# Optimization experiments

Measured on AMD Instinct MI355X. Metric: run time of the kernel, lower is better.

## Reference

```python
import jax, jax.numpy as jnp
import numpy as np

N = 200_000
E = 3_200_000
H = 24

def setup_inputs() -> dict:
    key = jax.random.key(0)
    ks = jax.random.split(key, 12)
    s = 1.0 / np.sqrt(H).astype(np.float32)
    u = lambda k, shape: jax.random.uniform(k, shape, jnp.float32, -s, s)
    return {
        "x": jax.random.normal(ks[0], (N,), jnp.float32),
        "h0": jax.random.normal(ks[1], (1, N, H), jnp.float32) * 0.1,
        "c0": jax.random.normal(ks[2], (1, N, H), jnp.float32) * 0.1,
        "edge_index": jax.random.randint(ks[3], (2, E), 0, N, dtype=jnp.int32),
        "w_ih": u(ks[4], (4 * H, 1)),
        "w_hh": u(ks[5], (4 * H, H)),
        "b_ih": u(ks[6], (4 * H,)),
        "b_hh": u(ks[7], (4 * H,)),
        "gcn_w": u(ks[8], (H, H)),
        "gcn_b": u(ks[9], (H,)),
        "lin_w": u(ks[10], (1, H)),
        "lin_b": u(ks[11], (1,)),
    }

def reference(x, h0, c0, edge_index, w_ih, w_hh, b_ih, b_hh, gcn_w, gcn_b, lin_w, lin_b):
    # --- LSTM single step (seq_len=1, batch=N, input_size=1, hidden=H) ---
    h_prev = h0[0]  # [N, H]
    c_prev = c0[0]  # [N, H]
    # gates in torch order: input, forget, cell(g), output
    gates = x[:, None] * w_ih[:, 0][None, :] + b_ih + h_prev @ w_hh.T + b_hh  # [N, 4H]
    i, f, g, o = jnp.split(gates, 4, axis=-1)
    i = jax.nn.sigmoid(i); f = jax.nn.sigmoid(f); o = jax.nn.sigmoid(o); g = jnp.tanh(g)
    c = f * c_prev + i * g
    h = o * jnp.tanh(c)  # [N, H] -- LSTM output == new hidden state

    # --- GCNConv(24,24): symmetric norm with self loops (PyG default) ---
    xw = h @ gcn_w.T  # [N, H]
    src, dst = edge_index[0], edge_index[1]
    deg = jax.ops.segment_sum(jnp.ones(src.shape, xw.dtype), dst, num_segments=N) + 1.0
    dinv = jax.lax.rsqrt(deg)                      # deg >= 1 due to self loops
    norm = dinv[src] * dinv[dst]                   # [E]
    msg = xw[src] * norm[:, None]                  # [E, H]
    agg = jax.ops.segment_sum(msg, dst, num_segments=N)
    agg = agg + xw * (dinv * dinv)[:, None]        # self-loop edges
    conv = agg + gcn_b                             # [N, H]

    # --- Linear(24,1) + elementwise gate ---
    out = (conv @ lin_w.T + lin_b).reshape(-1)     # [N]
    return x * out, h[None], c[None]
```

## Files before the change

kernel.cpp:

```cpp
#include <hip/hip_runtime.h>
#include <math.h>

#define H 24
#define B0 4096
#define B0_SHIFT 12
#define MAXNB 64
#define NBPAD 65
#define REP 4
#define P 8
#define CAP 70000
#define K1_EPB 4096
#define EPT (K1_EPB / 256)

__device__ __forceinline__ float sigmoidf_(float v) {
    return 1.0f / (1.0f + __expf(-v));
}
__device__ __forceinline__ float tanhf_(float v) {
    return 1.0f - 2.0f / (__expf(2.0f * v) + 1.0f);
}

__global__ void init_kernel(unsigned* __restrict__ cursors,
                            const float* __restrict__ gcn_w,
                            const float* __restrict__ gcn_b,
                            const float* __restrict__ lin_w,
                            const float* __restrict__ lin_b,
                            float* __restrict__ g, float* __restrict__ cb, int NB) {
    int t = threadIdx.x;
    if (t < H) {
        float acc = 0.0f;
        for (int j = 0; j < H; j++) acc = fmaf(lin_w[j], gcn_w[j * H + t], acc);
        g[t] = acc;
    }
    if (t == 32) {
        float c = lin_b[0];
        for (int j = 0; j < H; j++) c = fmaf(gcn_b[j], lin_w[j], c);
        *cb = c;
    }
    if (t < MAXNB) cursors[t] = (unsigned)t * CAP;
}

__global__ __launch_bounds__(256) void scatter_kernel(
    const int* __restrict__ src, const int* __restrict__ dst,
    unsigned* __restrict__ cursors, unsigned* __restrict__ pedge, int E, int NB)
{
    __shared__ unsigned cnt[REP * NBPAD];
    __shared__ unsigned rbase[MAXNB];
    __shared__ unsigned c3[MAXNB];
    int start = blockIdx.x * K1_EPB;
    int end   = start + K1_EPB; if (end > E) end = E;
    int rep = threadIdx.x & (REP - 1);

    for (int i = threadIdx.x; i < REP * NBPAD; i += 256) cnt[i] = 0;
    __syncthreads();

    unsigned dreg[EPT];
    #pragma unroll
    for (int q = 0; q < EPT; q++) {
        int e = start + q * 256 + threadIdx.x;
        if (e < end) {
            unsigned d = (unsigned)dst[e];
            dreg[q] = d;
            atomicAdd(&cnt[rep * NBPAD + (d >> B0_SHIFT)], 1u);
        }
    }
    __syncthreads();

    for (int i = threadIdx.x; i < NB; i += 256) {
        unsigned tot = cnt[i] + cnt[NBPAD + i] + cnt[2 * NBPAD + i] + cnt[3 * NBPAD + i];
        rbase[i] = tot ? atomicAdd(&cursors[i], tot) : 0u;
        c3[i] = 0;
    }
    __syncthreads();

    #pragma unroll
    for (int q = 0; q < EPT; q++) {
        int e = start + q * 256 + threadIdx.x;
        if (e < end) {
            unsigned d = dreg[q];
            unsigned b = d >> B0_SHIFT;
            unsigned slot = atomicAdd(&c3[b], 1u);
            unsigned idx  = rbase[b] + slot;
            if (idx < (b + 1u) * CAP)
                pedge[idx] = ((unsigned)src[e] << B0_SHIFT) | (d & (B0 - 1));
        }
    }
}

__global__ __launch_bounds__(256) void deghist_kernel(
    const unsigned* __restrict__ pedge, const unsigned* __restrict__ cursors,
    unsigned short* __restrict__ degp, int NB, int NPAD)
{
    __shared__ unsigned h[B0];
    int b = blockIdx.x % NB, p = blockIdx.x / NB;
    for (int i = threadIdx.x; i < B0; i += 256) h[i] = 0;
    __syncthreads();
    unsigned base = (unsigned)b * CAP;
    unsigned sz = cursors[b] - base; if (sz > CAP) sz = CAP;
    unsigned chunk = (sz + P - 1) / P;
    unsigned s0 = p * chunk;
    unsigned s1 = s0 + chunk; if (s1 > sz) s1 = sz;
    for (unsigned i = s0 + threadIdx.x; i < s1; i += 256)
        atomicAdd(&h[pedge[base + i] & (B0 - 1)], 1u);
    __syncthreads();
    unsigned short* out = degp + (size_t)p * NPAD + (size_t)b * B0;
    for (int i = threadIdx.x; i < B0; i += 256) out[i] = (unsigned short)h[i];
}

__global__ __launch_bounds__(256) void node_kernel(
    const float* __restrict__ x, const float* __restrict__ h0, const float* __restrict__ c0,
    const float* __restrict__ w_ih, const float* __restrict__ w_hh,
    const float* __restrict__ b_ih, const float* __restrict__ b_hh,
    const float* __restrict__ g, const unsigned short* __restrict__ degp, int NPAD,
    float* __restrict__ out_h, float* __restrict__ out_c,
    float* __restrict__ y, float* __restrict__ z, float* __restrict__ dinv, int N)
{
    __shared__ float ws[96 * 24];
    __shared__ float swih[96];
    __shared__ float sbs[96];
    __shared__ float sg[24];

    #pragma unroll 3
    for (int i = threadIdx.x; i < 96 * 24; i += 256) ws[i] = w_hh[i];
    if (threadIdx.x < 96) {
        swih[threadIdx.x] = w_ih[threadIdx.x];
        sbs[threadIdx.x]  = b_ih[threadIdx.x] + b_hh[threadIdx.x];
    } else if (threadIdx.x >= 128 && threadIdx.x < 152) {
        sg[threadIdx.x - 128] = g[threadIdx.x - 128];
    }
    __syncthreads();

    int tid = blockIdx.x * 256 + threadIdx.x;
    int pr  = tid >> 2;
    int n0  = pr * 2;
    if (n0 >= N) return;
    int n1  = n0 + 1;
    int t   = tid & 3;
    int k0  = 6 * t;

    float hp0[H], hp1[H];
    {
        const float4* a4 = (const float4*)(h0 + (size_t)n0 * H);
        const float4* b4 = (const float4*)(h0 + (size_t)n1 * H);
        #pragma unroll
        for (int q = 0; q < 6; q++) {
            float4 va = a4[q], vb = b4[q];
            hp0[4*q+0] = va.x; hp0[4*q+1] = va.y; hp0[4*q+2] = va.z; hp0[4*q+3] = va.w;
            hp1[4*q+0] = vb.x; hp1[4*q+1] = vb.y; hp1[4*q+2] = vb.z; hp1[4*q+3] = vb.w;
        }
    }
    float cp0[6], cp1[6];
    {
        const float2* a2 = (const float2*)(c0 + (size_t)n0 * H + k0);
        const float2* b2 = (const float2*)(c0 + (size_t)n1 * H + k0);
        #pragma unroll
        for (int q = 0; q < 3; q++) {
            float2 va = a2[q], vb = b2[q];
            cp0[2*q] = va.x; cp0[2*q+1] = va.y;
            cp1[2*q] = vb.x; cp1[2*q+1] = vb.y;
        }
    }
    float xv0 = x[n0], xv1 = x[n1];
    float yv0 = 0.0f, yv1 = 0.0f;

    #pragma unroll
    for (int i = 0; i < 6; i++) {
        int k = k0 + i;
        float bi = sbs[k], bf = sbs[k + 24], bg = sbs[k + 48], bo = sbs[k + 72];
        float wik = swih[k], wfk = swih[k + 24], wgk = swih[k + 48], wok = swih[k + 72];
        float gi0 = fmaf(xv0, wik, bi), gi1 = fmaf(xv1, wik, bi);
        float gf0 = fmaf(xv0, wfk, bf), gf1 = fmaf(xv1, wfk, bf);
        float gg0 = fmaf(xv0, wgk, bg), gg1 = fmaf(xv1, wgk, bg);
        float go0 = fmaf(xv0, wok, bo), go1 = fmaf(xv1, wok, bo);
        const float* w0 = ws + k * 24;
        #pragma unroll
        for (int c = 0; c < 6; c++) {
            float4 wi = *(const float4*)(w0 + 4*c);
            float4 wf = *(const float4*)(w0 + 576  + 4*c);
            float4 wg = *(const float4*)(w0 + 1152 + 4*c);
            float4 wo = *(const float4*)(w0 + 1728 + 4*c);
            float a0 = hp0[4*c+0], a1 = hp0[4*c+1], a2 = hp0[4*c+2], a3 = hp0[4*c+3];
            float d0 = hp1[4*c+0], d1 = hp1[4*c+1], d2 = hp1[4*c+2], d3 = hp1[4*c+3];
            gi0 = fmaf(a0, wi.x, gi0); gi0 = fmaf(a1, wi.y, gi0);
            gi0 = fmaf(a2, wi.z, gi0); gi0 = fmaf(a3, wi.w, gi0);
            gi1 = fmaf(d0, wi.x, gi1); gi1 = fmaf(d1, wi.y, gi1);
            gi1 = fmaf(d2, wi.z, gi1); gi1 = fmaf(d3, wi.w, gi1);
            gf0 = fmaf(a0, wf.x, gf0); gf0 = fmaf(a1, wf.y, gf0);
            gf0 = fmaf(a2, wf.z, gf0); gf0 = fmaf(a3, wf.w, gf0);
            gf1 = fmaf(d0, wf.x, gf1); gf1 = fmaf(d1, wf.y, gf1);
            gf1 = fmaf(d2, wf.z, gf1); gf1 = fmaf(d3, wf.w, gf1);
            gg0 = fmaf(a0, wg.x, gg0); gg0 = fmaf(a1, wg.y, gg0);
            gg0 = fmaf(a2, wg.z, gg0); gg0 = fmaf(a3, wg.w, gg0);
            gg1 = fmaf(d0, wg.x, gg1); gg1 = fmaf(d1, wg.y, gg1);
            gg1 = fmaf(d2, wg.z, gg1); gg1 = fmaf(d3, wg.w, gg1);
            go0 = fmaf(a0, wo.x, go0); go0 = fmaf(a1, wo.y, go0);
            go0 = fmaf(a2, wo.z, go0); go0 = fmaf(a3, wo.w, go0);
            go1 = fmaf(d0, wo.x, go1); go1 = fmaf(d1, wo.y, go1);
            go1 = fmaf(d2, wo.z, go1); go1 = fmaf(d3, wo.w, go1);
        }
        gi0 = sigmoidf_(gi0); gf0 = sigmoidf_(gf0); go0 = sigmoidf_(go0); gg0 = tanhf_(gg0);
        gi1 = sigmoidf_(gi1); gf1 = sigmoidf_(gf1); go1 = sigmoidf_(go1); gg1 = tanhf_(gg1);
        float c_0 = fmaf(gf0, cp0[i], gi0 * gg0);
        float c_1 = fmaf(gf1, cp1[i], gi1 * gg1);
        float h_0 = go0 * tanhf_(c_0);
        float h_1 = go1 * tanhf_(c_1);
        out_c[(size_t)n0 * H + k] = c_0;
        out_c[(size_t)n1 * H + k] = c_1;
        out_h[(size_t)n0 * H + k] = h_0;
        out_h[(size_t)n1 * H + k] = h_1;
        float gk = sg[k];
        yv0 = fmaf(h_0, gk, yv0);
        yv1 = fmaf(h_1, gk, yv1);
    }
    yv0 += __shfl_xor(yv0, 1); yv0 += __shfl_xor(yv0, 2);
    yv1 += __shfl_xor(yv1, 1); yv1 += __shfl_xor(yv1, 2);
    if (t < 2) {
        int n = (t == 0) ? n0 : n1;
        float yv = (t == 0) ? yv0 : yv1;
        unsigned dg = 0;
        #pragma unroll
        for (int p = 0; p < P; p++) dg += degp[(size_t)p * NPAD + n];
        float di = rsqrtf((float)dg + 1.0f);
        dinv[n] = di;
        y[n] = yv;
        z[n] = di * yv;
    }
}

__global__ __launch_bounds__(256) void acchist_kernel(
    const unsigned* __restrict__ pedge, const unsigned* __restrict__ cursors,
    const float* __restrict__ z, float* __restrict__ accp, int NB, int NPAD)
{
    __shared__ float h[B0];
    int b = blockIdx.x % NB, p = blockIdx.x / NB;
    for (int i = threadIdx.x; i < B0; i += 256) h[i] = 0.0f;
    __syncthreads();
    unsigned base = (unsigned)b * CAP;
    unsigned sz = cursors[b] - base; if (sz > CAP) sz = CAP;
    unsigned chunk = (sz + P - 1) / P;
    unsigned s0 = p * chunk;
    unsigned s1 = s0 + chunk; if (s1 > sz) s1 = sz;
    for (unsigned i = s0 + threadIdx.x; i < s1; i += 256) {
        unsigned v = pedge[base + i];
        atomicAdd(&h[v & (B0 - 1)], z[v >> B0_SHIFT]);
    }
    __syncthreads();
    float* out = accp + (size_t)p * NPAD + (size_t)b * B0;
    for (int i = threadIdx.x; i < B0; i += 256) out[i] = h[i];
}

__global__ __launch_bounds__(256) void final_kernel(
    const float* __restrict__ x, const float* __restrict__ accp, int NPAD,
    const float* __restrict__ y, const float* __restrict__ dinv,
    const float* __restrict__ cb, float* __restrict__ out, int N)
{
    int n = blockIdx.x * blockDim.x + threadIdx.x;
    if (n >= N) return;
    float a = 0.0f;
    #pragma unroll
    for (int p = 0; p < P; p++) a += accp[(size_t)p * NPAD + n];
    float di = dinv[n];
    float s  = di * a + di * di * y[n] + cb[0];
    out[n] = x[n] * s;
}

extern "C" void kernel_launch(void* const* d_in, const int* in_sizes, int n_in,
                              void* d_out, int out_size, void* d_ws, size_t ws_size,
                              hipStream_t stream) {
    const float* x     = (const float*)d_in[0];
    const float* h0    = (const float*)d_in[1];
    const float* c0    = (const float*)d_in[2];
    const int*   ei    = (const int*)d_in[3];
    const float* w_ih  = (const float*)d_in[4];
    const float* w_hh  = (const float*)d_in[5];
    const float* b_ih  = (const float*)d_in[6];
    const float* b_hh  = (const float*)d_in[7];
    const float* gcn_w = (const float*)d_in[8];
    const float* gcn_b = (const float*)d_in[9];
    const float* lin_w = (const float*)d_in[10];
    const float* lin_b = (const float*)d_in[11];

    const int N = in_sizes[0];
    const int E = in_sizes[3] / 2;
    const int* src = ei;
    const int* dst = ei + E;

    const int NB   = (N + B0 - 1) / B0;
    const int NPAD = NB * B0;

    float* out_gate = (float*)d_out;
    float* out_h    = out_gate + N;
    float* out_c    = out_h + (size_t)N * H;

    char* w = (char*)d_ws;
    unsigned*       pedge   = (unsigned*)w;       w += (size_t)NB * CAP * 4;
    unsigned short* degp    = (unsigned short*)w; w += (size_t)P * NPAD * 2;
    float*          accp    = (float*)w;          w += (size_t)P * NPAD * 4;
    float*          y       = (float*)w;          w += (size_t)N * 4;
    float*          zv      = (float*)w;          w += (size_t)N * 4;
    float*          dinv    = (float*)w;          w += (size_t)N * 4;
    float*          g       = (float*)w;          w += H * 4;
    float*          cb      = (float*)w;          w += 4;
    unsigned*       cursors = (unsigned*)w;       w += MAXNB * 4;

    init_kernel   <<<1, 64, 0, stream>>>(cursors, gcn_w, gcn_b, lin_w, lin_b, g, cb, NB);
    scatter_kernel<<<(E + K1_EPB - 1) / K1_EPB, 256, 0, stream>>>(src, dst, cursors,
                                                                  pedge, E, NB);
    deghist_kernel<<<NB * P, 256, 0, stream>>>(pedge, cursors, degp, NB, NPAD);
    node_kernel   <<<((size_t)(N / 2) * 4 + 255) / 256, 256, 0, stream>>>(
                       x, h0, c0, w_ih, w_hh, b_ih, b_hh, g, degp, NPAD,
                       out_h, out_c, y, zv, dinv, N);
    acchist_kernel<<<NB * P, 256, 0, stream>>>(pedge, cursors, zv, accp, NB, NPAD);
    final_kernel  <<<(N + 255) / 256, 256, 0, stream>>>(x, accp, NPAD, y, dinv, cb,
                                                        out_gate, N);
}
```

Baseline: 114.0 us.

## Fuse edge scatter and LSTM node work into one interleaved launch

Merges the edge-bucketing scatter kernel and the LSTM node kernel into a single launch. Every third block does scatter work and the remaining blocks do node work, with shared memory reused through a union. This lets the memory-bound scatter overlap the compute-heavy LSTM instead of running them in sequence. Because the node work no longer waits for the degree histogram, the dinv/z computation moves into a new small z_kernel that runs after deghist, which adds one launch and an extra pass over y.

```diff
diff --git a/kernel.cpp b/kernel.cpp
--- a/kernel.cpp
+++ b/kernel.cpp
@@ -39,97 +39,83 @@
     if (t < MAXNB) cursors[t] = (unsigned)t * CAP;
 }
 
-__global__ __launch_bounds__(256) void scatter_kernel(
+__global__ __launch_bounds__(256) void fused_kernel(
     const int* __restrict__ src, const int* __restrict__ dst,
-    unsigned* __restrict__ cursors, unsigned* __restrict__ pedge, int E, int NB)
-{
-    __shared__ unsigned cnt[REP * NBPAD];
-    __shared__ unsigned rbase[MAXNB];
-    __shared__ unsigned c3[MAXNB];
-    int start = blockIdx.x * K1_EPB;
-    int end   = start + K1_EPB; if (end > E) end = E;
-    int rep = threadIdx.x & (REP - 1);
-
-    for (int i = threadIdx.x; i < REP * NBPAD; i += 256) cnt[i] = 0;
-    __syncthreads();
-
-    unsigned dreg[EPT];
-    #pragma unroll
-    for (int q = 0; q < EPT; q++) {
-        int e = start + q * 256 + threadIdx.x;
-        if (e < end) {
-            unsigned d = (unsigned)dst[e];
-            dreg[q] = d;
-            atomicAdd(&cnt[rep * NBPAD + (d >> B0_SHIFT)], 1u);
-        }
-    }
-    __syncthreads();
-
-    for (int i = threadIdx.x; i < NB; i += 256) {
-        unsigned tot = cnt[i] + cnt[NBPAD + i] + cnt[2 * NBPAD + i] + cnt[3 * NBPAD + i];
-        rbase[i] = tot ? atomicAdd(&cursors[i], tot) : 0u;
-        c3[i] = 0;
-    }
-    __syncthreads();
-
-    #pragma unroll
-    for (int q = 0; q < EPT; q++) {
-        int e = start + q * 256 + threadIdx.x;
-        if (e < end) {
-            unsigned d = dreg[q];
-            unsigned b = d >> B0_SHIFT;
-            unsigned slot = atomicAdd(&c3[b], 1u);
-            unsigned idx  = rbase[b] + slot;
-            if (idx < (b + 1u) * CAP)
-                pedge[idx] = ((unsigned)src[e] << B0_SHIFT) | (d & (B0 - 1));
-        }
-    }
-}
-
-__global__ __launch_bounds__(256) void deghist_kernel(
-    const unsigned* __restrict__ pedge, const unsigned* __restrict__ cursors,
-    unsigned short* __restrict__ degp, int NB, int NPAD)
-{
-    __shared__ unsigned h[B0];
-    int b = blockIdx.x % NB, p = blockIdx.x / NB;
-    for (int i = threadIdx.x; i < B0; i += 256) h[i] = 0;
-    __syncthreads();
-    unsigned base = (unsigned)b * CAP;
-    unsigned sz = cursors[b] - base; if (sz > CAP) sz = CAP;
-    unsigned chunk = (sz + P - 1) / P;
-    unsigned s0 = p * chunk;
-    unsigned s1 = s0 + chunk; if (s1 > sz) s1 = sz;
-    for (unsigned i = s0 + threadIdx.x; i < s1; i += 256)
-        atomicAdd(&h[pedge[base + i] & (B0 - 1)], 1u);
-    __syncthreads();
-    unsigned short* out = degp + (size_t)p * NPAD + (size_t)b * B0;
-    for (int i = threadIdx.x; i < B0; i += 256) out[i] = (unsigned short)h[i];
-}
-
-__global__ __launch_bounds__(256) void node_kernel(
+    unsigned* __restrict__ cursors, unsigned* __restrict__ pedge, int E, int NB, int nscat,
     const float* __restrict__ x, const float* __restrict__ h0, const float* __restrict__ c0,
     const float* __restrict__ w_ih, const float* __restrict__ w_hh,
     const float* __restrict__ b_ih, const float* __restrict__ b_hh,
-    const float* __restrict__ g, const unsigned short* __restrict__ degp, int NPAD,
+    const float* __restrict__ g,
     float* __restrict__ out_h, float* __restrict__ out_c,
-    float* __restrict__ y, float* __restrict__ z, float* __restrict__ dinv, int N)
-{
-    __shared__ float ws[96 * 24];
-    __shared__ float swih[96];
-    __shared__ float sbs[96];
-    __shared__ float sg[24];
+    float* __restrict__ y, int N, int nnode)
+{
+    __shared__ union {
+        struct { unsigned cnt[REP * NBPAD]; unsigned rbase[MAXNB]; unsigned c3[MAXNB]; } s;
+        struct { float ws[96 * 24]; float swih[96]; float sbs[96]; float sg[24]; } n;
+    } u;
+
+    int bid = blockIdx.x;
+    int r = bid % 3, third = bid / 3;
+
+    if (r == 0 && third < nscat) {
+        int start = third * K1_EPB;
+        int end   = start + K1_EPB; if (end > E) end = E;
+        int rep = threadIdx.x & (REP - 1);
+
+        for (int i = threadIdx.x; i < REP * NBPAD; i += 256) u.s.cnt[i] = 0;
+        __syncthreads();
+
+        unsigned dreg[EPT];
+        #pragma unroll
+        for (int q = 0; q < EPT; q++) {
+            int e = start + q * 256 + threadIdx.x;
+            if (e < end) {
+                unsigned d = (unsigned)dst[e];
+                dreg[q] = d;
+                atomicAdd(&u.s.cnt[rep * NBPAD + (d >> B0_SHIFT)], 1u);
+            }
+        }
+        __syncthreads();
+
+        for (int i = threadIdx.x; i < NB; i += 256) {
+            unsigned tot = u.s.cnt[i] + u.s.cnt[NBPAD + i]
+                         + u.s.cnt[2 * NBPAD + i] + u.s.cnt[3 * NBPAD + i];
+            u.s.rbase[i] = tot ? atomicAdd(&cursors[i], tot) : 0u;
+            u.s.c3[i] = 0;
+        }
+        __syncthreads();
+
+        #pragma unroll
+        for (int q = 0; q < EPT; q++) {
+            int e = start + q * 256 + threadIdx.x;
+            if (e < end) {
+                unsigned d = dreg[q];
+                unsigned b = d >> B0_SHIFT;
+                unsigned slot = atomicAdd(&u.s.c3[b], 1u);
+                unsigned idx  = u.s.rbase[b] + slot;
+                if (idx < (b + 1u) * CAP)
+                    pedge[idx] = ((unsigned)src[e] << B0_SHIFT) | (d & (B0 - 1));
+            }
+        }
+        return;
+    }
+
+    int sb = (r == 0) ? third : third + 1;
+    if (sb > nscat) sb = nscat;
+    int nid = bid - sb;
+    if (nid >= nnode) return;
 
     #pragma unroll 3
-    for (int i = threadIdx.x; i < 96 * 24; i += 256) ws[i] = w_hh[i];
+    for (int i = threadIdx.x; i < 96 * 24; i += 256) u.n.ws[i] = w_hh[i];
     if (threadIdx.x < 96) {
-        swih[threadIdx.x] = w_ih[threadIdx.x];
-        sbs[threadIdx.x]  = b_ih[threadIdx.x] + b_hh[threadIdx.x];
+        u.n.swih[threadIdx.x] = w_ih[threadIdx.x];
+        u.n.sbs[threadIdx.x]  = b_ih[threadIdx.x] + b_hh[threadIdx.x];
     } else if (threadIdx.x >= 128 && threadIdx.x < 152) {
-        sg[threadIdx.x - 128] = g[threadIdx.x - 128];
-    }
-    __syncthreads();
-
-    int tid = blockIdx.x * 256 + threadIdx.x;
+        u.n.sg[threadIdx.x - 128] = g[threadIdx.x - 128];
+    }
+    __syncthreads();
+
+    int tid = nid * 256 + threadIdx.x;
     int pr  = tid >> 2;
     int n0  = pr * 2;
     if (n0 >= N) return;
@@ -165,13 +151,15 @@
     #pragma unroll
     for (int i = 0; i < 6; i++) {
         int k = k0 + i;
-        float bi = sbs[k], bf = sbs[k + 24], bg = sbs[k + 48], bo = sbs[k + 72];
-        float wik = swih[k], wfk = swih[k + 24], wgk = swih[k + 48], wok = swih[k + 72];
+        float bi = u.n.sbs[k], bf = u.n.sbs[k + 24];
+        float bg = u.n.sbs[k + 48], bo = u.n.sbs[k + 72];
+        float wik = u.n.swih[k], wfk = u.n.swih[k + 24];
+        float wgk = u.n.swih[k + 48], wok = u.n.swih[k + 72];
         float gi0 = fmaf(xv0, wik, bi), gi1 = fmaf(xv1, wik, bi);
         float gf0 = fmaf(xv0, wfk, bf), gf1 = fmaf(xv1, wfk, bf);
         float gg0 = fmaf(xv0, wgk, bg), gg1 = fmaf(xv1, wgk, bg);
         float go0 = fmaf(xv0, wok, bo), go1 = fmaf(xv1, wok, bo);
-        const float* w0 = ws + k * 24;
+        const float* w0 = u.n.ws + k * 24;
         #pragma unroll
         for (int c = 0; c < 6; c++) {
             float4 wi = *(const float4*)(w0 + 4*c);
@@ -207,23 +195,48 @@
         out_c[(size_t)n1 * H + k] = c_1;
         out_h[(size_t)n0 * H + k] = h_0;
         out_h[(size_t)n1 * H + k] = h_1;
-        float gk = sg[k];
+        float gk = u.n.sg[k];
         yv0 = fmaf(h_0, gk, yv0);
         yv1 = fmaf(h_1, gk, yv1);
     }
     yv0 += __shfl_xor(yv0, 1); yv0 += __shfl_xor(yv0, 2);
     yv1 += __shfl_xor(yv1, 1); yv1 += __shfl_xor(yv1, 2);
-    if (t < 2) {
-        int n = (t == 0) ? n0 : n1;
-        float yv = (t == 0) ? yv0 : yv1;
-        unsigned dg = 0;
-        #pragma unroll
-        for (int p = 0; p < P; p++) dg += degp[(size_t)p * NPAD + n];
-        float di = rsqrtf((float)dg + 1.0f);
-        dinv[n] = di;
-        y[n] = yv;
-        z[n] = di * yv;
-    }
+    if (t == 0) y[n0] = yv0;
+    if (t == 1) y[n1] = yv1;
+}
+
+__global__ __launch_bounds__(256) void deghist_kernel(
+    const unsigned* __restrict__ pedge, const unsigned* __restrict__ cursors,
+    unsigned short* __restrict__ degp, int NB, int NPAD)
+{
+    __shared__ unsigned h[B0];
+    int b = blockIdx.x % NB, p = blockIdx.x / NB;
+    for (int i = threadIdx.x; i < B0; i += 256) h[i] = 0;
+    __syncthreads();
+    unsigned base = (unsigned)b * CAP;
+    unsigned sz = cursors[b] - base; if (sz > CAP) sz = CAP;
+    unsigned chunk = (sz + P - 1) / P;
+    unsigned s0 = p * chunk;
+    unsigned s1 = s0 + chunk; if (s1 > sz) s1 = sz;
+    for (unsigned i = s0 + threadIdx.x; i < s1; i += 256)
+        atomicAdd(&h[pedge[base + i] & (B0 - 1)], 1u);
+    __syncthreads();
+    unsigned short* out = degp + (size_t)p * NPAD + (size_t)b * B0;
+    for (int i = threadIdx.x; i < B0; i += 256) out[i] = (unsigned short)h[i];
+}
+
+__global__ __launch_bounds__(256) void z_kernel(
+    const float* __restrict__ y, const unsigned short* __restrict__ degp, int NPAD,
+    float* __restrict__ dinv, float* __restrict__ z, int N)
+{
+    int n = blockIdx.x * 256 + threadIdx.x;
+    if (n >= N) return;
+    unsigned dg = 0;
+    #pragma unroll
+    for (int p = 0; p < P; p++) dg += degp[(size_t)p * NPAD + n];
+    float di = rsqrtf((float)dg + 1.0f);
+    dinv[n] = di;
+    z[n] = di * y[n];
 }
 
 __global__ __launch_bounds__(256) void acchist_kernel(
@@ -302,13 +315,17 @@
     float*          cb      = (float*)w;          w += 4;
     unsigned*       cursors = (unsigned*)w;       w += MAXNB * 4;
 
-    init_kernel   <<<1, 64, 0, stream>>>(cursors, gcn_w, gcn_b, lin_w, lin_b, g, cb, NB);
-    scatter_kernel<<<(E + K1_EPB - 1) / K1_EPB, 256, 0, stream>>>(src, dst, cursors,
-                                                                  pedge, E, NB);
+    const int NSCAT = (E + K1_EPB - 1) / K1_EPB;
+    const int NNODE = ((N / 2) * 4 + 255) / 256;
+    int total = NSCAT + NNODE;
+    if (NNODE <= 2 * NSCAT) total = 3 * NSCAT;
+
+    init_kernel  <<<1, 64, 0, stream>>>(cursors, gcn_w, gcn_b, lin_w, lin_b, g, cb, NB);
+    fused_kernel <<<total, 256, 0, stream>>>(src, dst, cursors, pedge, E, NB, NSCAT,
+                                             x, h0, c0, w_ih, w_hh, b_ih, b_hh, g,
+                                             out_h, out_c, y, N, NNODE);
     deghist_kernel<<<NB * P, 256, 0, stream>>>(pedge, cursors, degp, NB, NPAD);
-    node_kernel   <<<((size_t)(N / 2) * 4 + 255) / 256, 256, 0, stream>>>(
-                       x, h0, c0, w_ih, w_hh, b_ih, b_hh, g, degp, NPAD,
-                       out_h, out_c, y, zv, dinv, N);
+    z_kernel      <<<(N + 255) / 256, 256, 0, stream>>>(y, degp, NPAD, dinv, zv, N);
     acchist_kernel<<<NB * P, 256, 0, stream>>>(pedge, cursors, zv, accp, NB, NPAD);
     final_kernel  <<<(N + 255) / 256, 256, 0, stream>>>(x, accp, NPAD, y, dinv, cb,
                                                         out_gate, N);
```

After: 130.0 us. 14.0% more time.

## Spread scatter atomics, pad global cursors, move degree gather to separate kernel

Applied to the files above, without the earlier changes.

The scatter kernel now takes twice as many edges per block, uses 8 shared-memory count replicas, and keeps 4 per-replica slot counters with precomputed replica base offsets. This is meant to reduce LDS atomic contention and cut down on global cursor atomics. The global cursors are padded to separate cache lines to avoid false sharing between bins. The degree gather and dinv/z computation move out of the node kernel into a new lightweight z_kernel, so only one lane per node group no longer does the serialized degp reads. That adds an extra kernel launch and a round trip of y through memory.

```diff
diff --git a/kernel.cpp b/kernel.cpp
--- a/kernel.cpp
+++ b/kernel.cpp
@@ -6,10 +6,12 @@
 #define B0_SHIFT 12
 #define MAXNB 64
 #define NBPAD 65
-#define REP 4
+#define REP1 8
+#define REP3 4
 #define P 8
 #define CAP 70000
-#define K1_EPB 4096
+#define CSTRIDE 16
+#define K1_EPB 8192
 #define EPT (K1_EPB / 256)
 
 __device__ __forceinline__ float sigmoidf_(float v) {
@@ -36,21 +38,22 @@
         for (int j = 0; j < H; j++) c = fmaf(gcn_b[j], lin_w[j], c);
         *cb = c;
     }
-    if (t < MAXNB) cursors[t] = (unsigned)t * CAP;
+    if (t < MAXNB) cursors[t * CSTRIDE] = (unsigned)t * CAP;
 }
 
 __global__ __launch_bounds__(256) void scatter_kernel(
     const int* __restrict__ src, const int* __restrict__ dst,
     unsigned* __restrict__ cursors, unsigned* __restrict__ pedge, int E, int NB)
 {
-    __shared__ unsigned cnt[REP * NBPAD];
-    __shared__ unsigned rbase[MAXNB];
-    __shared__ unsigned c3[MAXNB];
+    __shared__ unsigned cnt[REP1 * NBPAD];
+    __shared__ unsigned rbase[REP3][MAXNB];
+    __shared__ unsigned c3[REP3 * NBPAD];
     int start = blockIdx.x * K1_EPB;
     int end   = start + K1_EPB; if (end > E) end = E;
-    int rep = threadIdx.x & (REP - 1);
-
-    for (int i = threadIdx.x; i < REP * NBPAD; i += 256) cnt[i] = 0;
+    int rep1 = threadIdx.x & (REP1 - 1);
+    int rep3 = rep1 >> 1;
+
+    for (int i = threadIdx.x; i < REP1 * NBPAD; i += 256) cnt[i] = 0;
     __syncthreads();
 
     unsigned dreg[EPT];
@@ -60,15 +63,24 @@
         if (e < end) {
             unsigned d = (unsigned)dst[e];
             dreg[q] = d;
-            atomicAdd(&cnt[rep * NBPAD + (d >> B0_SHIFT)], 1u);
+            atomicAdd(&cnt[rep1 * NBPAD + (d >> B0_SHIFT)], 1u);
         }
     }
     __syncthreads();
 
     for (int i = threadIdx.x; i < NB; i += 256) {
-        unsigned tot = cnt[i] + cnt[NBPAD + i] + cnt[2 * NBPAD + i] + cnt[3 * NBPAD + i];
-        rbase[i] = tot ? atomicAdd(&cursors[i], tot) : 0u;
-        c3[i] = 0;
+        unsigned c[REP1];
+        unsigned tot = 0;
+        #pragma unroll
+        for (int r = 0; r < REP1; r++) { c[r] = cnt[r * NBPAD + i]; tot += c[r]; }
+        unsigned gb = tot ? atomicAdd(&cursors[i * CSTRIDE], tot) : 0u;
+        unsigned s0 = c[0] + c[1], s1 = c[2] + c[3], s2 = c[4] + c[5];
+        rbase[0][i] = gb;
+        rbase[1][i] = gb + s0;
+        rbase[2][i] = gb + s0 + s1;
+        rbase[3][i] = gb + s0 + s1 + s2;
+        #pragma unroll
+        for (int r = 0; r < REP3; r++) c3[r * NBPAD + i] = 0;
     }
     __syncthreads();
 
@@ -78,8 +90,8 @@
         if (e < end) {
             unsigned d = dreg[q];
             unsigned b = d >> B0_SHIFT;
-            unsigned slot = atomicAdd(&c3[b], 1u);
-            unsigned idx  = rbase[b] + slot;
+            unsigned slot = atomicAdd(&c3[rep3 * NBPAD + b], 1u);
+            unsigned idx  = rbase[rep3][b] + slot;
             if (idx < (b + 1u) * CAP)
                 pedge[idx] = ((unsigned)src[e] << B0_SHIFT) | (d & (B0 - 1));
         }
@@ -95,7 +107,7 @@
     for (int i = threadIdx.x; i < B0; i += 256) h[i] = 0;
     __syncthreads();
     unsigned base = (unsigned)b * CAP;
-    unsigned sz = cursors[b] - base; if (sz > CAP) sz = CAP;
+    unsigned sz = cursors[b * CSTRIDE] - base; if (sz > CAP) sz = CAP;
     unsigned chunk = (sz + P - 1) / P;
     unsigned s0 = p * chunk;
     unsigned s1 = s0 + chunk; if (s1 > sz) s1 = sz;
@@ -110,9 +122,9 @@
     const float* __restrict__ x, const float* __restrict__ h0, const float* __restrict__ c0,
     const float* __restrict__ w_ih, const float* __restrict__ w_hh,
     const float* __restrict__ b_ih, const float* __restrict__ b_hh,
-    const float* __restrict__ g, const unsigned short* __restrict__ degp, int NPAD,
+    const float* __restrict__ g,
     float* __restrict__ out_h, float* __restrict__ out_c,
-    float* __restrict__ y, float* __restrict__ z, float* __restrict__ dinv, int N)
+    float* __restrict__ y, int N)
 {
     __shared__ float ws[96 * 24];
     __shared__ float swih[96];
@@ -213,17 +225,22 @@
     }
     yv0 += __shfl_xor(yv0, 1); yv0 += __shfl_xor(yv0, 2);
     yv1 += __shfl_xor(yv1, 1); yv1 += __shfl_xor(yv1, 2);
-    if (t < 2) {
-        int n = (t == 0) ? n0 : n1;
-        float yv = (t == 0) ? yv0 : yv1;
-        unsigned dg = 0;
-        #pragma unroll
-        for (int p = 0; p < P; p++) dg += degp[(size_t)p * NPAD + n];
-        float di = rsqrtf((float)dg + 1.0f);
-        dinv[n] = di;
-        y[n] = yv;
-        z[n] = di * yv;
-    }
+    if (t == 0) y[n0] = yv0;
+    if (t == 1) y[n1] = yv1;
+}
+
+__global__ __launch_bounds__(256) void z_kernel(
+    const float* __restrict__ y, const unsigned short* __restrict__ degp, int NPAD,
+    float* __restrict__ dinv, float* __restrict__ z, int N)
+{
+    int n = blockIdx.x * 256 + threadIdx.x;
+    if (n >= N) return;
+    unsigned dg = 0;
+    #pragma unroll
+    for (int p = 0; p < P; p++) dg += degp[(size_t)p * NPAD + n];
+    float di = rsqrtf((float)dg + 1.0f);
+    dinv[n] = di;
+    z[n] = di * y[n];
 }
 
 __global__ __launch_bounds__(256) void acchist_kernel(
@@ -235,7 +252,7 @@
     for (int i = threadIdx.x; i < B0; i += 256) h[i] = 0.0f;
     __syncthreads();
     unsigned base = (unsigned)b * CAP;
-    unsigned sz = cursors[b] - base; if (sz > CAP) sz = CAP;
+    unsigned sz = cursors[b * CSTRIDE] - base; if (sz > CAP) sz = CAP;
     unsigned chunk = (sz + P - 1) / P;
     unsigned s0 = p * chunk;
     unsigned s1 = s0 + chunk; if (s1 > sz) s1 = sz;
@@ -300,15 +317,15 @@
     float*          dinv    = (float*)w;          w += (size_t)N * 4;
     float*          g       = (float*)w;          w += H * 4;
     float*          cb      = (float*)w;          w += 4;
-    unsigned*       cursors = (unsigned*)w;       w += MAXNB * 4;
+    unsigned*       cursors = (unsigned*)w;       w += MAXNB * CSTRIDE * 4;
 
     init_kernel   <<<1, 64, 0, stream>>>(cursors, gcn_w, gcn_b, lin_w, lin_b, g, cb, NB);
     scatter_kernel<<<(E + K1_EPB - 1) / K1_EPB, 256, 0, stream>>>(src, dst, cursors,
                                                                   pedge, E, NB);
     deghist_kernel<<<NB * P, 256, 0, stream>>>(pedge, cursors, degp, NB, NPAD);
-    node_kernel   <<<((size_t)(N / 2) * 4 + 255) / 256, 256, 0, stream>>>(
-                       x, h0, c0, w_ih, w_hh, b_ih, b_hh, g, degp, NPAD,
-                       out_h, out_c, y, zv, dinv, N);
+    node_kernel   <<<((size_t)N * 2 + 255) / 256, 256, 0, stream>>>(
+                       x, h0, c0, w_ih, w_hh, b_ih, b_hh, g, out_h, out_c, y, N);
+    z_kernel      <<<(N + 255) / 256, 256, 0, stream>>>(y, degp, NPAD, dinv, zv, N);
     acchist_kernel<<<NB * P, 256, 0, stream>>>(pedge, cursors, zv, accp, NB, NPAD);
     final_kernel  <<<(N + 255) / 256, 256, 0, stream>>>(x, accp, NPAD, y, dinv, cb,
                                                         out_gate, N);
```

Result: slower. 119.3 us (+4.6%).
